# Optimization experiments

Measured on AMD Instinct MI355X. Metric: run time of the kernel, lower is better.

The kernel has to match this reference:

```python
import jax, jax.numpy as jnp
import numpy as np

EMBED_DIM = 1024
NUM_HEADS = 16
HEAD_DIM = EMBED_DIM // NUM_HEADS


def setup_inputs() -> dict:
    key = jax.random.key(0)
    kq, kk, kv, kw1, kw2 = jax.random.split(key, 5)
    B, S, D = 4, 2048, EMBED_DIM
    # xavier_uniform with gain=0.1
    lim_qkv = 0.1 * np.sqrt(6.0 / (D + 3 * D))
    lim_out = 0.1 * np.sqrt(6.0 / (D + D))
    return {
        "query": jax.random.normal(kq, (B, S, D), dtype=jnp.float32),
        "key": jax.random.normal(kk, (B, S, D), dtype=jnp.float32),
        "value": jax.random.normal(kv, (B, S, D), dtype=jnp.float32),
        "W_qkv": jax.random.uniform(kw1, (3 * D, D), jnp.float32, -lim_qkv, lim_qkv),
        "b_qkv": jnp.zeros((3 * D,), jnp.float32),
        "W_out": jax.random.uniform(kw2, (D, D), jnp.float32, -lim_out, lim_out),
        "b_out": jnp.zeros((D,), jnp.float32),
    }


def reference(query, key, value, W_qkv, b_qkv, W_out, b_out):
    # NOTE: the torch module computes Q,K,V all from `query` (self-attention);
    # `key`/`value` args are API placeholders and unused in the math.
    B, S, D = query.shape
    qkv = query @ W_qkv.T + b_qkv                     # [B,S,3D]
    qkv = qkv.reshape(B, S, 3, NUM_HEADS, HEAD_DIM)
    q = qkv[:, :, 0].transpose(0, 2, 1, 3)            # [B,H,S,hd]
    k = qkv[:, :, 1].transpose(0, 2, 1, 3)
    v = qkv[:, :, 2].transpose(0, 2, 1, 3)
    scale = 1.0 / np.sqrt(HEAD_DIM)
    scores = jnp.einsum("bhqd,bhkd->bhqk", q, k) * scale
    attn = jax.nn.softmax(scores, axis=-1)
    out = jnp.einsum("bhqk,bhkd->bhqd", attn, v)      # [B,H,S,hd]
    out = out.transpose(0, 2, 1, 3).reshape(B, S, D)
    return out @ W_out.T + b_out
```

## Files before the change

kernel.cpp:

```cpp
#include <hip/hip_runtime.h>

typedef __attribute__((ext_vector_type(8))) __bf16 bf16x8;
typedef __attribute__((ext_vector_type(4))) float f32x4;
typedef unsigned short u16;
typedef unsigned int u32;

__device__ __forceinline__ u16 f2bf(float x) {
  u32 u = __builtin_bit_cast(u32, x);
  u = (u + 0x7FFFu + ((u >> 16) & 1u)) >> 16;
  return (u16)u;
}

__global__ __launch_bounds__(256) void cvt3(
    const float* __restrict__ q, const float* __restrict__ w1,
    const float* __restrict__ w2, u16* __restrict__ oq, u16* __restrict__ ow1,
    u16* __restrict__ ow2) {
  int i = blockIdx.x * 256 + threadIdx.x;
  const float* in;
  u16* out;
  int base;
  if (i < 1048576) {
    in = q; out = oq; base = i;
  } else if (i < 1441792) {
    in = w1; out = ow1; base = i - 1048576;
  } else {
    in = w2; out = ow2; base = i - 1441792;
  }
  const float4* p = reinterpret_cast<const float4*>(in) + (size_t)base * 2;
  float4 a = p[0], b = p[1];
  uint4 r;
  r.x = (u32)f2bf(a.x) | ((u32)f2bf(a.y) << 16);
  r.y = (u32)f2bf(a.z) | ((u32)f2bf(a.w) << 16);
  r.z = (u32)f2bf(b.x) | ((u32)f2bf(b.y) << 16);
  r.w = (u32)f2bf(b.z) | ((u32)f2bf(b.w) << 16);
  reinterpret_cast<uint4*>(out)[base] = r;
}

__global__ __launch_bounds__(256) void gemm_qkv_bt(
    const u16* __restrict__ A, const u16* __restrict__ Bw,
    const float* __restrict__ bias, u16* __restrict__ Qh,
    u16* __restrict__ Kh, u16* __restrict__ Vt) {
  constexpr int K = 1024;
  __shared__ u16 As[128 * 64];
  __shared__ u16 Bs[128 * 64];
  const int tid = threadIdx.x;
  const int w = tid >> 6, l = tid & 63;
  const int kg = l >> 4, lr = l & 15;
  const int bid = blockIdx.x;
  const int wg = (bid & 7) * 192 + (bid >> 3);
  const int tm = wg / 24, tn = wg % 24;
  const int wr = w >> 1, wc = w & 1;

  const u16* Ab = A + (size_t)tm * 128 * K;
  const u16* Bb = Bw + (size_t)tn * 128 * K;

  const int sr0 = tid >> 3, sc0 = tid & 7;

#define GLL(SRC, DST)                                                   \
  __builtin_amdgcn_global_load_lds(                                     \
      (const __attribute__((address_space(1))) void*)(SRC),             \
      (__attribute__((address_space(3))) void*)(DST), 16, 0, 0)

  const f32x4 fz = {0.f, 0.f, 0.f, 0.f};
  f32x4 acc[4][4];
#pragma unroll
  for (int m = 0; m < 4; ++m)
#pragma unroll
    for (int n = 0; n < 4; ++n) acc[m][n] = fz;

  const int x7 = lr & 7;
  const int pc0 = (kg ^ x7) * 8;
  const int pc1 = ((kg + 4) ^ x7) * 8;

  for (int k0 = 0; k0 < K; k0 += 64) {
#pragma unroll
    for (int u = 0; u < 4; ++u) {
      const int s = u * 256 + tid;
      const int row = u * 32 + sr0;
      const int lc = sc0 ^ (row & 7);
      GLL(Ab + (size_t)row * K + k0 + lc * 8, As + s * 8);
      GLL(Bb + (size_t)row * K + k0 + lc * 8, Bs + s * 8);
    }
    asm volatile("s_waitcnt vmcnt(0)" ::: "memory");
    __syncthreads();
    bf16x8 a0[4], a1[4], b0[4], b1[4];
#pragma unroll
    for (int m = 0; m < 4; ++m) {
      const u16* rp = As + (wr * 64 + m * 16 + lr) * 64;
      a0[m] = *(const bf16x8*)(rp + pc0);
      a1[m] = *(const bf16x8*)(rp + pc1);
    }
#pragma unroll
    for (int n = 0; n < 4; ++n) {
      const u16* rp = Bs + (wc * 64 + n * 16 + lr) * 64;
      b0[n] = *(const bf16x8*)(rp + pc0);
      b1[n] = *(const bf16x8*)(rp + pc1);
    }
#pragma unroll
    for (int m = 0; m < 4; ++m)
#pragma unroll
      for (int n = 0; n < 4; ++n) {
        acc[m][n] =
            __builtin_amdgcn_mfma_f32_16x16x32_bf16(a0[m], b0[n], acc[m][n], 0, 0, 0);
        acc[m][n] =
            __builtin_amdgcn_mfma_f32_16x16x32_bf16(a1[m], b1[n], acc[m][n], 0, 0, 0);
      }
    __syncthreads();
  }

#pragma unroll
  for (int m = 0; m < 4; ++m) {
    const int i0 = tm * 128 + wr * 64 + m * 16 + kg * 4;
    const int b = i0 >> 11, s0 = i0 & 2047;
#pragma unroll
    for (int n = 0; n < 4; ++n) {
      const int jc = tn * 128 + wc * 64 + n * 16 + lr;
      const float bs = bias[jc];
      const int sel = jc >> 10, hh = (jc >> 6) & 15, d = jc & 63;
      if (sel == 0) {
        u16* qp = Qh + ((size_t)((b * 16 + hh) * 2048 + s0)) * 64 + d;
#pragma unroll
        for (int j = 0; j < 4; ++j)
          qp[(size_t)j * 64] = f2bf((acc[m][n][j] + bs) * 0.18033688f);
      } else if (sel == 1) {
        u16* kp = Kh + ((size_t)((b * 16 + hh) * 2048 + s0)) * 64 + d;
#pragma unroll
        for (int j = 0; j < 4; ++j) kp[(size_t)j * 64] = f2bf(acc[m][n][j] + bs);
      } else {
        ushort4 vv;
        vv.x = f2bf(acc[m][n][0] + bs);
        vv.y = f2bf(acc[m][n][1] + bs);
        vv.z = f2bf(acc[m][n][2] + bs);
        vv.w = f2bf(acc[m][n][3] + bs);
        *(ushort4*)(Vt + ((size_t)((b * 16 + hh) * 64 + d)) * 2048 + s0) = vv;
      }
    }
  }
#undef GLL
}

__global__ __launch_bounds__(256) void gemm_out_bt(
    const u16* __restrict__ A, const u16* __restrict__ Bw,
    const float* __restrict__ bias, float* __restrict__ Cout) {
  constexpr int N = 1024, K = 1024;
  __shared__ u16 As[128 * 64];
  __shared__ u16 Bs[128 * 64];
  const int tid = threadIdx.x;
  const int w = tid >> 6, l = tid & 63;
  const int kg = l >> 4, lr = l & 15;
  const int bid = blockIdx.x;
  const int wg = (bid & 7) * 64 + (bid >> 3);
  const int tm = wg >> 3, tn = wg & 7;
  const int wr = w >> 1, wc = w & 1;

  const u16* Ab = A + (size_t)tm * 128 * K;
  const u16* Bb = Bw + (size_t)tn * 128 * K;

  const int sr0 = tid >> 3, sc0 = tid & 7;

#define GLL(SRC, DST)                                                   \
  __builtin_amdgcn_global_load_lds(                                     \
      (const __attribute__((address_space(1))) void*)(SRC),             \
      (__attribute__((address_space(3))) void*)(DST), 16, 0, 0)

  const f32x4 fz = {0.f, 0.f, 0.f, 0.f};
  f32x4 acc[4][4];
#pragma unroll
  for (int m = 0; m < 4; ++m)
#pragma unroll
    for (int n = 0; n < 4; ++n) acc[m][n] = fz;

  const int x7 = lr & 7;
  const int pc0 = (kg ^ x7) * 8;
  const int pc1 = ((kg + 4) ^ x7) * 8;

  for (int k0 = 0; k0 < K; k0 += 64) {
#pragma unroll
    for (int u = 0; u < 4; ++u) {
      const int s = u * 256 + tid;
      const int row = u * 32 + sr0;
      const int lc = sc0 ^ (row & 7);
      GLL(Ab + (size_t)row * K + k0 + lc * 8, As + s * 8);
      GLL(Bb + (size_t)row * K + k0 + lc * 8, Bs + s * 8);
    }
    asm volatile("s_waitcnt vmcnt(0)" ::: "memory");
    __syncthreads();
    bf16x8 a0[4], a1[4], b0[4], b1[4];
#pragma unroll
    for (int m = 0; m < 4; ++m) {
      const u16* rp = As + (wr * 64 + m * 16 + lr) * 64;
      a0[m] = *(const bf16x8*)(rp + pc0);
      a1[m] = *(const bf16x8*)(rp + pc1);
    }
#pragma unroll
    for (int n = 0; n < 4; ++n) {
      const u16* rp = Bs + (wc * 64 + n * 16 + lr) * 64;
      b0[n] = *(const bf16x8*)(rp + pc0);
      b1[n] = *(const bf16x8*)(rp + pc1);
    }
#pragma unroll
    for (int m = 0; m < 4; ++m)
#pragma unroll
      for (int n = 0; n < 4; ++n) {
        acc[m][n] =
            __builtin_amdgcn_mfma_f32_16x16x32_bf16(a0[m], b0[n], acc[m][n], 0, 0, 0);
        acc[m][n] =
            __builtin_amdgcn_mfma_f32_16x16x32_bf16(a1[m], b1[n], acc[m][n], 0, 0, 0);
      }
    __syncthreads();
  }

#pragma unroll
  for (int m = 0; m < 4; ++m) {
    const int i0 = tm * 128 + wr * 64 + m * 16 + kg * 4;
#pragma unroll
    for (int n = 0; n < 4; ++n) {
      const int jc = tn * 128 + wc * 64 + n * 16 + lr;
      const float bs = bias[jc];
#pragma unroll
      for (int j = 0; j < 4; ++j)
        Cout[(size_t)(i0 + j) * N + jc] = acc[m][n][j] + bs;
    }
  }
#undef GLL
}

__global__ __launch_bounds__(256, 4) void attn_kernel(
    const u16* __restrict__ Qh, const u16* __restrict__ Kh,
    const u16* __restrict__ Vt, u16* __restrict__ Aout) {
  __shared__ alignas(16) u16 Kl[2][4096];
  __shared__ alignas(16) u16 Vl[2][4096];
  const int tid = threadIdx.x;
  const int w = tid >> 6, l = tid & 63;
  const int kg = l >> 4, lq = l & 15;
  const int bid = blockIdx.x;
  const int wgi = (bid & 7) * 128 + (bid >> 3);
  const int bh = wgi >> 4, qt = wgi & 15;
  const int qbase = qt * 128 + w * 32;

  const u16* Qb = Qh + ((size_t)(bh * 2048 + qbase + lq)) * 64;
  const bf16x8 aq00 = *(const bf16x8*)(Qb + kg * 8);
  const bf16x8 aq01 = *(const bf16x8*)(Qb + 32 + kg * 8);
  const bf16x8 aq10 = *(const bf16x8*)(Qb + 16 * 64 + kg * 8);
  const bf16x8 aq11 = *(const bf16x8*)(Qb + 16 * 64 + 32 + kg * 8);

  const u16* Kb = Kh + (size_t)bh * 2048 * 64;
  const u16* Vb = Vt + (size_t)bh * 64 * 2048;

  const int r7K = 4 * (lq >> 3) + (lq & 3);
  const int rowbK = 8 * ((lq >> 2) & 1) + r7K;
  const int ckK0 = (kg ^ r7K) * 8;
  const int ckK1 = ((kg + 4) ^ r7K) * 8;
  const int r7V = lq & 7;
  const int ckV0 = (kg ^ r7V) * 8;
  const int ckV1 = ((kg + 4) ^ r7V) * 8;

  bf16x8 vone;
#pragma unroll
  for (int i = 0; i < 8; ++i) vone[i] = (__bf16)1.0f;

  const f32x4 fz = {0.f, 0.f, 0.f, 0.f};
  f32x4 on0[4] = {fz, fz, fz, fz};
  f32x4 on1[4] = {fz, fz, fz, fz};
  f32x4 ls0 = fz, ls1 = fz;

#define STAGE_KV(buf, kc)                                                        \
  {                                                                              \
    {                                                                            \
      const int s_ = tid, row_ = s_ >> 3, c_ = s_ & 7;                           \
      const int sw_ = (c_ ^ (row_ & 7)) * 8;                                     \
      const int srow_ = (row_ & ~20) | ((row_ & 4) << 2) | ((row_ & 16) >> 2);   \
      __builtin_amdgcn_global_load_lds(                                          \
          (const __attribute__((address_space(1))) void*)(Kb + (size_t)((kc) + srow_) * 64 + sw_), \
          (__attribute__((address_space(3))) void*)(&Kl[buf][s_ * 8]), 16, 0, 0);\
      __builtin_amdgcn_global_load_lds(                                          \
          (const __attribute__((address_space(1))) void*)(Vb + (size_t)row_ * 2048 + (kc) + sw_),  \
          (__attribute__((address_space(3))) void*)(&Vl[buf][s_ * 8]), 16, 0, 0);\
    }                                                                            \
    {                                                                            \
      const int s_ = 256 + tid, row_ = s_ >> 3, c_ = s_ & 7;                     \
      const int sw_ = (c_ ^ (row_ & 7)) * 8;                                     \
      const int srow_ = (row_ & ~20) | ((row_ & 4) << 2) | ((row_ & 16) >> 2);   \
      __builtin_amdgcn_global_load_lds(                                          \
          (const __attribute__((address_space(1))) void*)(Kb + (size_t)((kc) + srow_) * 64 + sw_), \
          (__attribute__((address_space(3))) void*)(&Kl[buf][s_ * 8]), 16, 0, 0);\
      __builtin_amdgcn_global_load_lds(                                          \
          (const __attribute__((address_space(1))) void*)(Vb + (size_t)row_ * 2048 + (kc) + sw_),  \
          (__attribute__((address_space(3))) void*)(&Vl[buf][s_ * 8]), 16, 0, 0);\
    }                                                                            \
  }

  STAGE_KV(0, 0);
  asm volatile("s_waitcnt vmcnt(0)" ::: "memory");
  __syncthreads();

  int cur = 0;
  for (int kc = 0; kc < 2048; kc += 64) {
    if (kc + 64 < 2048) STAGE_KV(cur ^ 1, kc + 64);
    const u16* Klc = Kl[cur];
    const u16* Vlc = Vl[cur];

    f32x4 st0[4], st1[4];
    __builtin_amdgcn_s_setprio(1);
#pragma unroll
    for (int t = 0; t < 4; ++t) {
      const int ro = (rowbK + ((t >> 1) * 32 + (t & 1) * 16)) * 64;
      bf16x8 k0 = *(const bf16x8*)(Klc + ro + ckK0);
      bf16x8 k1 = *(const bf16x8*)(Klc + ro + ckK1);
      f32x4 z0 = fz, z1 = fz;
      z0 = __builtin_amdgcn_mfma_f32_16x16x32_bf16(k0, aq00, z0, 0, 0, 0);
      z0 = __builtin_amdgcn_mfma_f32_16x16x32_bf16(k1, aq01, z0, 0, 0, 0);
      z1 = __builtin_amdgcn_mfma_f32_16x16x32_bf16(k0, aq10, z1, 0, 0, 0);
      z1 = __builtin_amdgcn_mfma_f32_16x16x32_bf16(k1, aq11, z1, 0, 0, 0);
      st0[t] = z0;
      st1[t] = z1;
    }
    __builtin_amdgcn_s_setprio(0);

    bf16x8 pa00, pa01, pa10, pa11;
#pragma unroll
    for (int j = 0; j < 4; ++j) {
      pa00[j] = (__bf16)__builtin_amdgcn_exp2f(st0[0][j]);
      pa00[4 + j] = (__bf16)__builtin_amdgcn_exp2f(st0[1][j]);
      pa01[j] = (__bf16)__builtin_amdgcn_exp2f(st0[2][j]);
      pa01[4 + j] = (__bf16)__builtin_amdgcn_exp2f(st0[3][j]);
      pa10[j] = (__bf16)__builtin_amdgcn_exp2f(st1[0][j]);
      pa10[4 + j] = (__bf16)__builtin_amdgcn_exp2f(st1[1][j]);
      pa11[j] = (__bf16)__builtin_amdgcn_exp2f(st1[2][j]);
      pa11[4 + j] = (__bf16)__builtin_amdgcn_exp2f(st1[3][j]);
    }

    __builtin_amdgcn_s_setprio(1);
    ls0 = __builtin_amdgcn_mfma_f32_16x16x32_bf16(pa00, vone, ls0, 0, 0, 0);
    ls0 = __builtin_amdgcn_mfma_f32_16x16x32_bf16(pa01, vone, ls0, 0, 0, 0);
    ls1 = __builtin_amdgcn_mfma_f32_16x16x32_bf16(pa10, vone, ls1, 0, 0, 0);
    ls1 = __builtin_amdgcn_mfma_f32_16x16x32_bf16(pa11, vone, ls1, 0, 0, 0);
#pragma unroll
    for (int n = 0; n < 4; ++n) {
      const int ro = (n * 16 + lq) * 64;
      bf16x8 v0 = *(const bf16x8*)(Vlc + ro + ckV0);
      bf16x8 v1 = *(const bf16x8*)(Vlc + ro + ckV1);
      on0[n] = __builtin_amdgcn_mfma_f32_16x16x32_bf16(pa00, v0, on0[n], 0, 0, 0);
      on0[n] = __builtin_amdgcn_mfma_f32_16x16x32_bf16(pa01, v1, on0[n], 0, 0, 0);
      on1[n] = __builtin_amdgcn_mfma_f32_16x16x32_bf16(pa10, v0, on1[n], 0, 0, 0);
      on1[n] = __builtin_amdgcn_mfma_f32_16x16x32_bf16(pa11, v1, on1[n], 0, 0, 0);
    }
    __builtin_amdgcn_s_setprio(0);

    asm volatile("s_waitcnt vmcnt(0)" ::: "memory");
    __syncthreads();
    cur ^= 1;
  }

  const int b = bh >> 4, h = bh & 15;
  {
    u16* Ob = Aout + (size_t)(b * 2048 + qbase + kg * 4) * 1024 + h * 64 + lq;
#pragma unroll
    for (int j = 0; j < 4; ++j) {
      float inv = 1.f / ls0[j];
#pragma unroll
      for (int n = 0; n < 4; ++n)
        Ob[(size_t)j * 1024 + n * 16] = f2bf(on0[n][j] * inv);
    }
  }
  {
    u16* Ob = Aout + (size_t)(b * 2048 + qbase + 16 + kg * 4) * 1024 + h * 64 + lq;
#pragma unroll
    for (int j = 0; j < 4; ++j) {
      float inv = 1.f / ls1[j];
#pragma unroll
      for (int n = 0; n < 4; ++n)
        Ob[(size_t)j * 1024 + n * 16] = f2bf(on1[n][j] * inv);
    }
  }
}

extern "C" void kernel_launch(void* const* d_in, const int* in_sizes, int n_in,
                              void* d_out, int out_size, void* d_ws, size_t ws_size,
                              hipStream_t stream) {
  const float* query = (const float*)d_in[0];
  const float* Wqkv = (const float*)d_in[3];
  const float* bqkv = (const float*)d_in[4];
  const float* Wout = (const float*)d_in[5];
  const float* bout = (const float*)d_in[6];
  float* out = (float*)d_out;

  char* ws = (char*)d_ws;
  u16* qx = (u16*)(ws);
  u16* wqkvb = (u16*)(ws + 16777216);
  u16* woutb = (u16*)(ws + 23068672);
  u16* Qh = (u16*)(ws + 25165824);
  u16* Kh = (u16*)(ws + 41943040);
  u16* Vt = (u16*)(ws + 58720256);
  u16* attn = qx;

  cvt3<<<6144, 256, 0, stream>>>(query, Wqkv, Wout, qx, wqkvb, woutb);

  gemm_qkv_bt<<<1536, 256, 0, stream>>>(qx, wqkvb, bqkv, Qh, Kh, Vt);
  attn_kernel<<<1024, 256, 0, stream>>>(Qh, Kh, Vt, attn);
  gemm_out_bt<<<512, 256, 0, stream>>>(attn, woutb, bout, out);
}
```

Baseline: 173.0 us.

## Double-buffer GEMM LDS tiles with K-step of 32 and merge GEMM kernels

```diff
diff --git a/kernel.cpp b/kernel.cpp
--- a/kernel.cpp
+++ b/kernel.cpp
@@ -36,30 +36,50 @@
   reinterpret_cast<uint4*>(out)[base] = r;
 }
 
-__global__ __launch_bounds__(256) void gemm_qkv_bt(
+template <int MODE>
+__global__ __launch_bounds__(256) void gemm_db(
     const u16* __restrict__ A, const u16* __restrict__ Bw,
     const float* __restrict__ bias, u16* __restrict__ Qh,
-    u16* __restrict__ Kh, u16* __restrict__ Vt) {
+    u16* __restrict__ Kh, u16* __restrict__ Vt, float* __restrict__ Cout) {
   constexpr int K = 1024;
-  __shared__ u16 As[128 * 64];
-  __shared__ u16 Bs[128 * 64];
+  constexpr int NT = 32;
+  constexpr int TN = (MODE == 0) ? 24 : 8;
+  __shared__ u16 As[2][4096];
+  __shared__ u16 Bs[2][4096];
   const int tid = threadIdx.x;
   const int w = tid >> 6, l = tid & 63;
   const int kg = l >> 4, lr = l & 15;
   const int bid = blockIdx.x;
-  const int wg = (bid & 7) * 192 + (bid >> 3);
-  const int tm = wg / 24, tn = wg % 24;
+  const int wg = (bid & 7) * (TN * 8) + (bid >> 3);
+  const int tm = wg / TN, tn = wg % TN;
   const int wr = w >> 1, wc = w & 1;
 
   const u16* Ab = A + (size_t)tm * 128 * K;
   const u16* Bb = Bw + (size_t)tn * 128 * K;
 
-  const int sr0 = tid >> 3, sc0 = tid & 7;
+  const int sr0 = tid >> 2, sc0 = tid & 3;
 
 #define GLL(SRC, DST)                                                   \
   __builtin_amdgcn_global_load_lds(                                     \
       (const __attribute__((address_space(1))) void*)(SRC),             \
       (__attribute__((address_space(3))) void*)(DST), 16, 0, 0)
+#define STAGE(BUF, KOFF)                                                \
+  {                                                                     \
+    {                                                                   \
+      const int row_ = sr0;                                             \
+      const int lc_ = sc0 ^ (row_ & 3);                                 \
+      GLL(Ab + (size_t)row_ * K + (KOFF) + lc_ * 8, As[BUF] + tid * 8); \
+      GLL(Bb + (size_t)row_ * K + (KOFF) + lc_ * 8, Bs[BUF] + tid * 8); \
+    }                                                                   \
+    {                                                                   \
+      const int row_ = 64 + sr0;                                        \
+      const int lc_ = sc0 ^ (row_ & 3);                                 \
+      GLL(Ab + (size_t)row_ * K + (KOFF) + lc_ * 8,                     \
+          As[BUF] + 2048 + tid * 8);                                    \
+      GLL(Bb + (size_t)row_ * K + (KOFF) + lc_ * 8,                     \
+          Bs[BUF] + 2048 + tid * 8);                                    \
+    }                                                                   \
+  }
 
   const f32x4 fz = {0.f, 0.f, 0.f, 0.f};
   f32x4 acc[4][4];
@@ -68,161 +88,81 @@
 #pragma unroll
     for (int n = 0; n < 4; ++n) acc[m][n] = fz;
 
-  const int x7 = lr & 7;
-  const int pc0 = (kg ^ x7) * 8;
-  const int pc1 = ((kg + 4) ^ x7) * 8;
-
-  for (int k0 = 0; k0 < K; k0 += 64) {
-#pragma unroll
-    for (int u = 0; u < 4; ++u) {
-      const int s = u * 256 + tid;
-      const int row = u * 32 + sr0;
-      const int lc = sc0 ^ (row & 7);
-      GLL(Ab + (size_t)row * K + k0 + lc * 8, As + s * 8);
-      GLL(Bb + (size_t)row * K + k0 + lc * 8, Bs + s * 8);
-    }
+  const int pc = (kg ^ (lr & 3)) * 8;
+
+  STAGE(0, 0);
+  asm volatile("s_waitcnt vmcnt(0)" ::: "memory");
+  __syncthreads();
+
+  int cur = 0;
+  for (int t = 0; t < NT; ++t) {
+    if (t + 1 < NT) STAGE(cur ^ 1, (t + 1) * 32);
+    const u16* Asc = As[cur];
+    const u16* Bsc = Bs[cur];
+    bf16x8 a[4], b[4];
+#pragma unroll
+    for (int m = 0; m < 4; ++m)
+      a[m] = *(const bf16x8*)(Asc + (wr * 64 + m * 16 + lr) * 32 + pc);
+#pragma unroll
+    for (int n = 0; n < 4; ++n)
+      b[n] = *(const bf16x8*)(Bsc + (wc * 64 + n * 16 + lr) * 32 + pc);
+#pragma unroll
+    for (int m = 0; m < 4; ++m)
+#pragma unroll
+      for (int n = 0; n < 4; ++n)
+        acc[m][n] =
+            __builtin_amdgcn_mfma_f32_16x16x32_bf16(a[m], b[n], acc[m][n], 0, 0, 0);
     asm volatile("s_waitcnt vmcnt(0)" ::: "memory");
     __syncthreads();
-    bf16x8 a0[4], a1[4], b0[4], b1[4];
+    cur ^= 1;
+  }
+
+  if (MODE == 0) {
 #pragma unroll
     for (int m = 0; m < 4; ++m) {
-      const u16* rp = As + (wr * 64 + m * 16 + lr) * 64;
-      a0[m] = *(const bf16x8*)(rp + pc0);
-      a1[m] = *(const bf16x8*)(rp + pc1);
-    }
-#pragma unroll
-    for (int n = 0; n < 4; ++n) {
-      const u16* rp = Bs + (wc * 64 + n * 16 + lr) * 64;
-      b0[n] = *(const bf16x8*)(rp + pc0);
-      b1[n] = *(const bf16x8*)(rp + pc1);
-    }
-#pragma unroll
-    for (int m = 0; m < 4; ++m)
+      const int i0 = tm * 128 + wr * 64 + m * 16 + kg * 4;
+      const int b = i0 >> 11, s0 = i0 & 2047;
 #pragma unroll
       for (int n = 0; n < 4; ++n) {
-        acc[m][n] =
-            __builtin_amdgcn_mfma_f32_16x16x32_bf16(a0[m], b0[n], acc[m][n], 0, 0, 0);
-        acc[m][n] =
-            __builtin_amdgcn_mfma_f32_16x16x32_bf16(a1[m], b1[n], acc[m][n], 0, 0, 0);
+        const int jc = tn * 128 + wc * 64 + n * 16 + lr;
+        const float bs = bias[jc];
+        const int sel = jc >> 10, hh = (jc >> 6) & 15, d = jc & 63;
+        if (sel == 0) {
+          u16* qp = Qh + ((size_t)((b * 16 + hh) * 2048 + s0)) * 64 + d;
+#pragma unroll
+          for (int j = 0; j < 4; ++j)
+            qp[(size_t)j * 64] = f2bf((acc[m][n][j] + bs) * 0.18033688f);
+        } else if (sel == 1) {
+          u16* kp = Kh + ((size_t)((b * 16 + hh) * 2048 + s0)) * 64 + d;
+#pragma unroll
+          for (int j = 0; j < 4; ++j)
+            kp[(size_t)j * 64] = f2bf(acc[m][n][j] + bs);
+        } else {
+          ushort4 vv;
+          vv.x = f2bf(acc[m][n][0] + bs);
+          vv.y = f2bf(acc[m][n][1] + bs);
+          vv.z = f2bf(acc[m][n][2] + bs);
+          vv.w = f2bf(acc[m][n][3] + bs);
+          *(ushort4*)(Vt + ((size_t)((b * 16 + hh) * 64 + d)) * 2048 + s0) = vv;
+        }
       }
-    __syncthreads();
-  }
-
-#pragma unroll
-  for (int m = 0; m < 4; ++m) {
-    const int i0 = tm * 128 + wr * 64 + m * 16 + kg * 4;
-    const int b = i0 >> 11, s0 = i0 & 2047;
-#pragma unroll
-    for (int n = 0; n < 4; ++n) {
-      const int jc = tn * 128 + wc * 64 + n * 16 + lr;
-      const float bs = bias[jc];
-      const int sel = jc >> 10, hh = (jc >> 6) & 15, d = jc & 63;
-      if (sel == 0) {
-        u16* qp = Qh + ((size_t)((b * 16 + hh) * 2048 + s0)) * 64 + d;
+    }
+  } else {
+#pragma unroll
+    for (int m = 0; m < 4; ++m) {
+      const int i0 = tm * 128 + wr * 64 + m * 16 + kg * 4;
+#pragma unroll
+      for (int n = 0; n < 4; ++n) {
+        const int jc = tn * 128 + wc * 64 + n * 16 + lr;
+        const float bs = bias[jc];
 #pragma unroll
         for (int j = 0; j < 4; ++j)
-          qp[(size_t)j * 64] = f2bf((acc[m][n][j] + bs) * 0.18033688f);
-      } else if (sel == 1) {
-        u16* kp = Kh + ((size_t)((b * 16 + hh) * 2048 + s0)) * 64 + d;
-#pragma unroll
-        for (int j = 0; j < 4; ++j) kp[(size_t)j * 64] = f2bf(acc[m][n][j] + bs);
-      } else {
-        ushort4 vv;
-        vv.x = f2bf(acc[m][n][0] + bs);
-        vv.y = f2bf(acc[m][n][1] + bs);
-        vv.z = f2bf(acc[m][n][2] + bs);
-        vv.w = f2bf(acc[m][n][3] + bs);
-        *(ushort4*)(Vt + ((size_t)((b * 16 + hh) * 64 + d)) * 2048 + s0) = vv;
+          Cout[(size_t)(i0 + j) * 1024 + jc] = acc[m][n][j] + bs;
       }
     }
   }
 #undef GLL
-}
-
-__global__ __launch_bounds__(256) void gemm_out_bt(
-    const u16* __restrict__ A, const u16* __restrict__ Bw,
-    const float* __restrict__ bias, float* __restrict__ Cout) {
-  constexpr int N = 1024, K = 1024;
-  __shared__ u16 As[128 * 64];
-  __shared__ u16 Bs[128 * 64];
-  const int tid = threadIdx.x;
-  const int w = tid >> 6, l = tid & 63;
-  const int kg = l >> 4, lr = l & 15;
-  const int bid = blockIdx.x;
-  const int wg = (bid & 7) * 64 + (bid >> 3);
-  const int tm = wg >> 3, tn = wg & 7;
-  const int wr = w >> 1, wc = w & 1;
-
-  const u16* Ab = A + (size_t)tm * 128 * K;
-  const u16* Bb = Bw + (size_t)tn * 128 * K;
-
-  const int sr0 = tid >> 3, sc0 = tid & 7;
-
-#define GLL(SRC, DST)                                                   \
-  __builtin_amdgcn_global_load_lds(                                     \
-      (const __attribute__((address_space(1))) void*)(SRC),             \
-      (__attribute__((address_space(3))) void*)(DST), 16, 0, 0)
-
-  const f32x4 fz = {0.f, 0.f, 0.f, 0.f};
-  f32x4 acc[4][4];
-#pragma unroll
-  for (int m = 0; m < 4; ++m)
-#pragma unroll
-    for (int n = 0; n < 4; ++n) acc[m][n] = fz;
-
-  const int x7 = lr & 7;
-  const int pc0 = (kg ^ x7) * 8;
-  const int pc1 = ((kg + 4) ^ x7) * 8;
-
-  for (int k0 = 0; k0 < K; k0 += 64) {
-#pragma unroll
-    for (int u = 0; u < 4; ++u) {
-      const int s = u * 256 + tid;
-      const int row = u * 32 + sr0;
-      const int lc = sc0 ^ (row & 7);
-      GLL(Ab + (size_t)row * K + k0 + lc * 8, As + s * 8);
-      GLL(Bb + (size_t)row * K + k0 + lc * 8, Bs + s * 8);
-    }
-    asm volatile("s_waitcnt vmcnt(0)" ::: "memory");
-    __syncthreads();
-    bf16x8 a0[4], a1[4], b0[4], b1[4];
-#pragma unroll
-    for (int m = 0; m < 4; ++m) {
-      const u16* rp = As + (wr * 64 + m * 16 + lr) * 64;
-      a0[m] = *(const bf16x8*)(rp + pc0);
-      a1[m] = *(const bf16x8*)(rp + pc1);
-    }
-#pragma unroll
-    for (int n = 0; n < 4; ++n) {
-      const u16* rp = Bs + (wc * 64 + n * 16 + lr) * 64;
-      b0[n] = *(const bf16x8*)(rp + pc0);
-      b1[n] = *(const bf16x8*)(rp + pc1);
-    }
-#pragma unroll
-    for (int m = 0; m < 4; ++m)
-#pragma unroll
-      for (int n = 0; n < 4; ++n) {
-        acc[m][n] =
-            __builtin_amdgcn_mfma_f32_16x16x32_bf16(a0[m], b0[n], acc[m][n], 0, 0, 0);
-        acc[m][n] =
-            __builtin_amdgcn_mfma_f32_16x16x32_bf16(a1[m], b1[n], acc[m][n], 0, 0, 0);
-      }
-    __syncthreads();
-  }
-
-#pragma unroll
-  for (int m = 0; m < 4; ++m) {
-    const int i0 = tm * 128 + wr * 64 + m * 16 + kg * 4;
-#pragma unroll
-    for (int n = 0; n < 4; ++n) {
-      const int jc = tn * 128 + wc * 64 + n * 16 + lr;
-      const float bs = bias[jc];
-#pragma unroll
-      for (int j = 0; j < 4; ++j)
-        Cout[(size_t)(i0 + j) * N + jc] = acc[m][n][j] + bs;
-    }
-  }
-#undef GLL
+#undef STAGE
 }
 
 __global__ __launch_bounds__(256, 4) void attn_kernel(
@@ -396,7 +336,8 @@
 
   cvt3<<<6144, 256, 0, stream>>>(query, Wqkv, Wout, qx, wqkvb, woutb);
 
-  gemm_qkv_bt<<<1536, 256, 0, stream>>>(qx, wqkvb, bqkv, Qh, Kh, Vt);
+  gemm_db<0><<<1536, 256, 0, stream>>>(qx, wqkvb, bqkv, Qh, Kh, Vt, nullptr);
   attn_kernel<<<1024, 256, 0, stream>>>(Qh, Kh, Vt, attn);
-  gemm_out_bt<<<512, 256, 0, stream>>>(attn, woutb, bout, out);
-}
+  gemm_db<1><<<512, 256, 0, stream>>>(attn, woutb, bout, nullptr, nullptr,
+                                      nullptr, out);
+}
```

Measured after the change: 182.9 us. 5.8% more time.
